# Kernel tuning notes

Measured on AMD Instinct MI355X. Metric: run time of the kernel, lower is better.

## Reference

```python
import jax, jax.numpy as jnp
import numpy as np

# Pauli-Z expectation table: sign of bit w in 4-bit index (wire 0 = MSB, axis order q0..q3)
_idx = np.arange(16)
_bits = (_idx[None, :] >> (3 - np.arange(4))[:, None]) & 1
_Z_TABLE = (1.0 - 2.0 * _bits).astype(np.float32)  # (4, 16)


def _apply_ry(state, theta, wire):
    # state: (N, 2,2,2,2) real amplitudes; RY = [[c,-s],[s,c]], c=cos(t/2), s=sin(t/2)
    ax = 1 + wire
    c = jnp.cos(theta / 2)
    s = jnp.sin(theta / 2)
    st = jnp.moveaxis(state, ax, 1)
    s0, s1 = st[:, 0], st[:, 1]
    st = jnp.stack([c * s0 - s * s1, s * s0 + c * s1], axis=1)
    return jnp.moveaxis(st, 1, ax)


def _apply_cnot(state, control, target):
    # flips the target axis on the control==1 slice (assumes target > control)
    ac, at = 1 + control, 1 + target
    s0 = jnp.take(state, 0, axis=ac)
    s1 = jnp.flip(jnp.take(state, 1, axis=ac), axis=at - 1)
    return jnp.stack([s0, s1], axis=ac)


def setup_inputs() -> dict:
    key = jax.random.key(0)
    ks = jax.random.split(key, 8)
    B = 8192
    x = jax.random.uniform(ks[0], (B, 1, 28, 28), dtype=jnp.float32)
    conv_w = jax.random.normal(ks[1], (4, 1, 2, 2), dtype=jnp.float32) * 0.5
    conv_b = jax.random.normal(ks[2], (4,), dtype=jnp.float32) * 0.1
    bn_gamma = jnp.ones((4,), jnp.float32)
    bn_beta = jnp.zeros((4,), jnp.float32)
    bn_mean = jnp.zeros((4,), jnp.float32)
    bn_var = jnp.ones((4,), jnp.float32)
    shortcut_weight = jnp.float32(1.0)
    theta = jax.random.normal(ks[3], (8,), dtype=jnp.float32)  # 8 trainable RY angles
    lin_w = jax.random.normal(ks[4], (10, 784), dtype=jnp.float32) * 0.03
    lin_b = jnp.zeros((10,), jnp.float32)
    log_scale = jnp.float32(1.0)
    return {"x": x, "conv_w": conv_w, "conv_b": conv_b, "bn_gamma": bn_gamma,
            "bn_beta": bn_beta, "bn_mean": bn_mean, "bn_var": bn_var,
            "shortcut_weight": shortcut_weight, "theta": theta,
            "lin_w": lin_w, "lin_b": lin_b, "log_scale": log_scale}


def reference(x, conv_w, conv_b, bn_gamma, bn_beta, bn_mean, bn_var,
              shortcut_weight, theta, lin_w, lin_b, log_scale):
    B = x.shape[0]
    # classical shortcut: conv(1->4, k2, s2) + BN (eval mode, running stats)
    sc = jax.lax.conv_general_dilated(
        x, conv_w, window_strides=(2, 2), padding='VALID',
        dimension_numbers=('NCHW', 'OIHW', 'NCHW')) + conv_b[None, :, None, None]
    sc = (sc - bn_mean[None, :, None, None]) * jax.lax.rsqrt(bn_var[None, :, None, None] + 1e-5)
    sc = sc * bn_gamma[None, :, None, None] + bn_beta[None, :, None, None]
    sc = sc.reshape(B, -1)  # (B, 784) channel-major, matches torch .view

    # extract 2x2 patches in (r, c) scan order -> (B*196, 4) with order [tl, tr, bl, br]
    img = x.reshape(B, 28, 28)
    patches = img.reshape(B, 14, 2, 14, 2).transpose(0, 1, 3, 2, 4).reshape(B * 196, 4)

    # RY encoding of |0000>: product state, amplitudes [cos(v/2), sin(v/2)] per wire
    half = patches * 0.5
    e = jnp.stack([jnp.cos(half), jnp.sin(half)], axis=-1)  # (N, 4, 2)
    state = jnp.einsum('na,nb,nc,nd->nabcd', e[:, 0], e[:, 1], e[:, 2], e[:, 3])

    # parameterized circuit: RY layer, CNOT(0,1), CNOT(2,3), RY layer
    for w in range(4):
        state = _apply_ry(state, theta[w], w)
    state = _apply_cnot(state, 0, 1)
    state = _apply_cnot(state, 2, 3)
    for w in range(4):
        state = _apply_ry(state, theta[4 + w], w)

    # <Z_w> expectations (real amplitudes -> probs = state**2)
    probs = (state ** 2).reshape(-1, 16)        # (B*196, 16)
    meas = probs @ jnp.asarray(_Z_TABLE).T      # (B*196, 4)
    qfeat = meas.reshape(B, 196 * 4)            # cat order: patch-major, wires inner

    feat = shortcut_weight * sc + qfeat
    logits = (feat @ lin_w.T + lin_b) * log_scale  # dropout is identity in eval
    return jax.nn.log_softmax(logits, axis=-1)
```

## Files before the change

kernel.cpp:

```cpp
#include <hip/hip_runtime.h>
#include <hip/hip_fp16.h>
#include <math.h>

#define BLOCK 256
#define WAVES 4
#define IPW   2
#define LWS   792
#define FEATS 792

typedef _Float16 h2v __attribute__((ext_vector_type(2)));

__device__ __forceinline__ float dot2h(unsigned a, unsigned b, float c) {
#if __has_builtin(__builtin_amdgcn_fdot2)
    return __builtin_amdgcn_fdot2(__builtin_bit_cast(h2v, a),
                                  __builtin_bit_cast(h2v, b), c, false);
#else
    h2v xa = __builtin_bit_cast(h2v, a), yb = __builtin_bit_cast(h2v, b);
    return c + (float)xa[0] * (float)yb[0] + (float)xa[1] * (float)yb[1];
#endif
}

__device__ __forceinline__ unsigned packh(float a, float b) {
    __half2 h = __float22half2_rn(make_float2(a, b));
    return __builtin_bit_cast(unsigned, h);
}

__global__ __launch_bounds__(BLOCK) void quanv_fused2(
    const float* __restrict__ x,
    const float* __restrict__ conv_w,
    const float* __restrict__ conv_b,
    const float* __restrict__ bn_gamma,
    const float* __restrict__ bn_beta,
    const float* __restrict__ bn_mean,
    const float* __restrict__ bn_var,
    const float* __restrict__ sw_p,
    const float* __restrict__ theta,
    const float* __restrict__ lin_w,
    const float* __restrict__ lin_b,
    const float* __restrict__ log_scale_p,
    float* __restrict__ out)
{
    __shared__ __half lw[10 * LWS];
    __shared__ __half feat[WAVES][FEATS];

    const int t = threadIdx.x;
    const int lane = t & 63, wv = t >> 6;
    __half* fw = &feat[wv][0];

    for (int g = t * 4; g < 7840; g += BLOCK * 4) {
        float4 v = *(const float4*)(lin_w + g);
        int k = g / 784, f = g - k * 784;
        uint2 pk;
        pk.x = packh(v.x, v.y);
        pk.y = packh(v.z, v.w);
        *(uint2*)&lw[k * LWS + f] = pk;
    }

    const float sw = sw_p[0];
    const float ls = log_scale_p[0];
    float wf[4][4], bf[4];
#pragma unroll
    for (int c = 0; c < 4; ++c) {
        float scale = bn_gamma[c] * rsqrtf(bn_var[c] + 1e-5f);
        float sws = sw * scale;
#pragma unroll
        for (int k = 0; k < 4; ++k) wf[c][k] = sws * conv_w[c * 4 + k];
        bf[c] = sw * (scale * (conv_b[c] - bn_mean[c]) + bn_beta[c]);
    }
    const float th0 = theta[0], th1 = theta[1], th2 = theta[2], th3 = theta[3];
    float s4, c4, s5, c5, s6, c6, s7, c7;
    __sincosf(0.5f * theta[4], &s4, &c4);
    __sincosf(0.5f * theta[5], &s5, &c5);
    __sincosf(0.5f * theta[6], &s6, &c6);
    __sincosf(0.5f * theta[7], &s7, &c7);

    auto pair_meas = [&](float xa, float xb, float tha, float thb,
                         float sE, float cE, float sF, float cF,
                         float& mA, float& mB) {
        float sA, cA, sB, cB;
        __sincosf(0.5f * (xa + tha), &sA, &cA);
        __sincosf(0.5f * (xb + thb), &sB, &cB);
        float cc = cA * cB, ss = sA * sB, cs = cA * sB, sc_ = sA * cB;
        float u0 = cE * cc - sE * ss;
        float u1 = cE * cs - sE * sc_;
        float u2 = sE * cc + cE * ss;
        float u3 = sE * cs + cE * sc_;
        float v0 = cF * u0 - sF * u1, v1 = sF * u0 + cF * u1;
        float v2 = cF * u2 - sF * u3, v3 = sF * u2 + cF * u3;
        mA = u0 * u0 + u1 * u1 - u2 * u2 - u3 * u3;
        mB = v0 * v0 - v1 * v1 + v2 * v2 - v3 * v3;
    };

    float2 px[8];
    auto load_pix = [&](int img) {
        const float* xb = x + (size_t)img * 784;
#pragma unroll
        for (int j = 0; j < 4; ++j) {
            int p = lane + 64 * j; if (p > 195) p = 195;
            int i = p / 14, jj = p - i * 14;
            px[2 * j]     = *(const float2*)(xb + (2 * i) * 28 + 2 * jj);
            px[2 * j + 1] = *(const float2*)(xb + (2 * i + 1) * 28 + 2 * jj);
        }
    };

    const int img0 = (blockIdx.x * WAVES + wv) * IPW;
    load_pix(img0);

    for (int it = 0; it < IPW; ++it) {
        const int img = img0 + it;
        unsigned q0[4], q1[4];

#pragma unroll
        for (int j = 0; j < 3; ++j) {
            const int p = lane + 64 * j;
            float x00 = px[2 * j].x, x01 = px[2 * j].y;
            float x10 = px[2 * j + 1].x, x11 = px[2 * j + 1].y;
            float m0, m1, m2, m3;
            pair_meas(x00, x01, th0, th1, s4, c4, s5, c5, m0, m1);
            pair_meas(x10, x11, th2, th3, s6, c6, s7, c7, m2, m3);
            q0[j] = packh(m0, m1);
            q1[j] = packh(m2, m3);
#pragma unroll
            for (int c = 0; c < 4; ++c)
                fw[c * 196 + p] = __float2half(
                    wf[c][0] * x00 + wf[c][1] * x01 +
                    wf[c][2] * x10 + wf[c][3] * x11 + bf[c]);
        }
        if (lane < 4) {
            const int p = lane + 192;
            float x00 = px[6].x, x01 = px[6].y;
            float x10 = px[7].x, x11 = px[7].y;
            float m0, m1, m2, m3;
            pair_meas(x00, x01, th0, th1, s4, c4, s5, c5, m0, m1);
            pair_meas(x10, x11, th2, th3, s6, c6, s7, c7, m2, m3);
            q0[3] = packh(m0, m1);
            q1[3] = packh(m2, m3);
#pragma unroll
            for (int c = 0; c < 4; ++c)
                fw[c * 196 + p] = __float2half(
                    wf[c][0] * x00 + wf[c][1] * x01 +
                    wf[c][2] * x10 + wf[c][3] * x11 + bf[c]);
        }

        if (it + 1 < IPW) load_pix(img + 1);

        __syncthreads();

#pragma unroll
        for (int j = 0; j < 3; ++j) {
            const int p = lane + 64 * j;
            uint2 v = *(uint2*)&fw[4 * p];
            __half2 a0 = __builtin_bit_cast(__half2, v.x);
            __half2 a1 = __builtin_bit_cast(__half2, v.y);
            a0 = __hadd2(a0, __builtin_bit_cast(__half2, q0[j]));
            a1 = __hadd2(a1, __builtin_bit_cast(__half2, q1[j]));
            v.x = __builtin_bit_cast(unsigned, a0);
            v.y = __builtin_bit_cast(unsigned, a1);
            *(uint2*)&fw[4 * p] = v;
        }
        if (lane < 4) {
            const int p = lane + 192;
            uint2 v = *(uint2*)&fw[4 * p];
            __half2 a0 = __builtin_bit_cast(__half2, v.x);
            __half2 a1 = __builtin_bit_cast(__half2, v.y);
            a0 = __hadd2(a0, __builtin_bit_cast(__half2, q0[3]));
            a1 = __hadd2(a1, __builtin_bit_cast(__half2, q1[3]));
            v.x = __builtin_bit_cast(unsigned, a0);
            v.y = __builtin_bit_cast(unsigned, a1);
            *(uint2*)&fw[4 * p] = v;
        }

        __syncthreads();

        float acc = 0.f;
        if (lane < 60) {
            const int k = lane / 6, c = lane - k * 6;
            const int start = c * 136;
            const int nit = (c == 5) ? 13 : 17;
            const uint4* fp = (const uint4*)&fw[start];
            const uint4* wp = (const uint4*)&lw[k * LWS + start];
            for (int i = 0; i < nit; ++i) {
                uint4 a = fp[i], b = wp[i];
                acc = dot2h(a.x, b.x, acc);
                acc = dot2h(a.y, b.y, acc);
                acc = dot2h(a.z, b.z, acc);
                acc = dot2h(a.w, b.w, acc);
            }
        }
        float s1 = acc + __shfl_down(acc, 1);
        float s2 = s1 + __shfl_down(s1, 2);
        float tot = s2 + __shfl_down(s1, 4);

        float logit = 0.f;
        if (lane < 60 && lane % 6 == 0)
            logit = (tot + lin_b[lane / 6]) * ls;

        float m = -1e30f;
        float lg;
#pragma unroll
        for (int kk = 0; kk < 10; ++kk) {
            float v = __shfl(logit, kk * 6);
            m = fmaxf(m, v);
        }
        float ssum = 0.f;
#pragma unroll
        for (int kk = 0; kk < 10; ++kk) {
            float v = __shfl(logit, kk * 6);
            ssum += __expf(v - m);
        }
        const float lse = m + __logf(ssum);
        lg = __shfl(logit, 6 * lane);
        if (lane < 10) out[(size_t)img * 10 + lane] = lg - lse;

        __syncthreads();
    }
}

extern "C" void kernel_launch(void* const* d_in, const int* in_sizes, int n_in,
                              void* d_out, int out_size, void* d_ws, size_t ws_size,
                              hipStream_t stream) {
    const float* x         = (const float*)d_in[0];
    const float* conv_w    = (const float*)d_in[1];
    const float* conv_b    = (const float*)d_in[2];
    const float* bn_gamma  = (const float*)d_in[3];
    const float* bn_beta   = (const float*)d_in[4];
    const float* bn_mean   = (const float*)d_in[5];
    const float* bn_var    = (const float*)d_in[6];
    const float* sw        = (const float*)d_in[7];
    const float* theta     = (const float*)d_in[8];
    const float* lin_w     = (const float*)d_in[9];
    const float* lin_b     = (const float*)d_in[10];
    const float* log_scale = (const float*)d_in[11];
    float* out = (float*)d_out;

    const int B = in_sizes[0] / 784;
    dim3 grid(B / (WAVES * IPW)), block(BLOCK);
    hipLaunchKernelGGL(quanv_fused2, grid, block, 0, stream,
                       x, conv_w, conv_b, bn_gamma, bn_beta, bn_mean, bn_var,
                       sw, theta, lin_w, lin_b, log_scale, out);
}
```

Measured before the change: 19.99 us.

## Process both images per wave concurrently with one block barrier

Blocks grow to 8 waves, and each wave handles its two images in parallel rather than in a loop. Both images' pixels are loaded up front, before the lin_w staging, and each image gets its own shared feature buffer. The three block-wide barriers per image become a wave-local lgkmcnt wait plus a single __syncthreads. Weight reads from shared memory are reused across both images' dot products. The aim is to cut barrier stalls and serialized latency, at the cost of more registers and shared memory per block, which may reduce occupancy.

```diff
diff --git a/kernel.cpp b/kernel.cpp
--- a/kernel.cpp
+++ b/kernel.cpp
@@ -2,9 +2,8 @@
 #include <hip/hip_fp16.h>
 #include <math.h>
 
-#define BLOCK 256
-#define WAVES 4
-#define IPW   2
+#define BLOCK 512
+#define WVS   8
 #define LWS   792
 #define FEATS 792
 
@@ -25,7 +24,9 @@
     return __builtin_bit_cast(unsigned, h);
 }
 
-__global__ __launch_bounds__(BLOCK) void quanv_fused2(
+#define WAVE_LGKM() asm volatile("s_waitcnt lgkmcnt(0)" ::: "memory")
+
+__global__ __launch_bounds__(BLOCK, 4) void quanv_fused3(
     const float* __restrict__ x,
     const float* __restrict__ conv_w,
     const float* __restrict__ conv_b,
@@ -41,11 +42,31 @@
     float* __restrict__ out)
 {
     __shared__ __half lw[10 * LWS];
-    __shared__ __half feat[WAVES][FEATS];
+    __shared__ __half feat[WVS][2][FEATS];
 
     const int t = threadIdx.x;
     const int lane = t & 63, wv = t >> 6;
-    __half* fw = &feat[wv][0];
+    __half* fw0 = &feat[wv][0][0];
+    __half* fw1 = &feat[wv][1][0];
+
+    const int img0 = (blockIdx.x * WVS + wv) * 2;
+    const int img1 = img0 + 1;
+
+    float2 px0[8], px1[8];
+    {
+        const float* xb0 = x + (size_t)img0 * 784;
+        const float* xb1 = x + (size_t)img1 * 784;
+#pragma unroll
+        for (int j = 0; j < 4; ++j) {
+            int p = lane + 64 * j; if (p > 195) p = 195;
+            int i = p / 14, jj = p - i * 14;
+            const int o0 = (2 * i) * 28 + 2 * jj, o1 = o0 + 28;
+            px0[2 * j]     = *(const float2*)(xb0 + o0);
+            px0[2 * j + 1] = *(const float2*)(xb0 + o1);
+            px1[2 * j]     = *(const float2*)(xb1 + o0);
+            px1[2 * j + 1] = *(const float2*)(xb1 + o1);
+        }
+    }
 
     for (int g = t * 4; g < 7840; g += BLOCK * 4) {
         float4 v = *(const float4*)(lin_w + g);
@@ -91,25 +112,8 @@
         mB = v0 * v0 - v1 * v1 + v2 * v2 - v3 * v3;
     };
 
-    float2 px[8];
-    auto load_pix = [&](int img) {
-        const float* xb = x + (size_t)img * 784;
-#pragma unroll
-        for (int j = 0; j < 4; ++j) {
-            int p = lane + 64 * j; if (p > 195) p = 195;
-            int i = p / 14, jj = p - i * 14;
-            px[2 * j]     = *(const float2*)(xb + (2 * i) * 28 + 2 * jj);
-            px[2 * j + 1] = *(const float2*)(xb + (2 * i + 1) * 28 + 2 * jj);
-        }
-    };
-
-    const int img0 = (blockIdx.x * WAVES + wv) * IPW;
-    load_pix(img0);
-
-    for (int it = 0; it < IPW; ++it) {
-        const int img = img0 + it;
-        unsigned q0[4], q1[4];
-
+    unsigned qa0[4], qa1[4], qb0[4], qb1[4];
+    auto pass1 = [&](const float2* px, __half* fw, unsigned* q0, unsigned* q1) {
 #pragma unroll
         for (int j = 0; j < 3; ++j) {
             const int p = lane + 64 * j;
@@ -141,13 +145,16 @@
                     wf[c][0] * x00 + wf[c][1] * x01 +
                     wf[c][2] * x10 + wf[c][3] * x11 + bf[c]);
         }
-
-        if (it + 1 < IPW) load_pix(img + 1);
-
-        __syncthreads();
-
-#pragma unroll
-        for (int j = 0; j < 3; ++j) {
+    };
+    pass1(px0, fw0, qa0, qa1);
+    pass1(px1, fw1, qb0, qb1);
+
+    WAVE_LGKM();
+
+    auto pass2 = [&](__half* fw, const unsigned* q0, const unsigned* q1) {
+#pragma unroll
+        for (int j = 0; j < 4; ++j) {
+            if (j == 3 && lane >= 4) break;
             const int p = lane + 64 * j;
             uint2 v = *(uint2*)&fw[4 * p];
             __half2 a0 = __builtin_bit_cast(__half2, v.x);
@@ -158,61 +165,66 @@
             v.y = __builtin_bit_cast(unsigned, a1);
             *(uint2*)&fw[4 * p] = v;
         }
-        if (lane < 4) {
-            const int p = lane + 192;
-            uint2 v = *(uint2*)&fw[4 * p];
-            __half2 a0 = __builtin_bit_cast(__half2, v.x);
-            __half2 a1 = __builtin_bit_cast(__half2, v.y);
-            a0 = __hadd2(a0, __builtin_bit_cast(__half2, q0[3]));
-            a1 = __hadd2(a1, __builtin_bit_cast(__half2, q1[3]));
-            v.x = __builtin_bit_cast(unsigned, a0);
-            v.y = __builtin_bit_cast(unsigned, a1);
-            *(uint2*)&fw[4 * p] = v;
-        }
-
-        __syncthreads();
-
-        float acc = 0.f;
-        if (lane < 60) {
-            const int k = lane / 6, c = lane - k * 6;
-            const int start = c * 136;
-            const int nit = (c == 5) ? 13 : 17;
-            const uint4* fp = (const uint4*)&fw[start];
-            const uint4* wp = (const uint4*)&lw[k * LWS + start];
-            for (int i = 0; i < nit; ++i) {
-                uint4 a = fp[i], b = wp[i];
-                acc = dot2h(a.x, b.x, acc);
-                acc = dot2h(a.y, b.y, acc);
-                acc = dot2h(a.z, b.z, acc);
-                acc = dot2h(a.w, b.w, acc);
-            }
-        }
-        float s1 = acc + __shfl_down(acc, 1);
-        float s2 = s1 + __shfl_down(s1, 2);
-        float tot = s2 + __shfl_down(s1, 4);
-
-        float logit = 0.f;
-        if (lane < 60 && lane % 6 == 0)
-            logit = (tot + lin_b[lane / 6]) * ls;
-
-        float m = -1e30f;
-        float lg;
-#pragma unroll
-        for (int kk = 0; kk < 10; ++kk) {
-            float v = __shfl(logit, kk * 6);
-            m = fmaxf(m, v);
-        }
-        float ssum = 0.f;
-#pragma unroll
-        for (int kk = 0; kk < 10; ++kk) {
-            float v = __shfl(logit, kk * 6);
-            ssum += __expf(v - m);
-        }
-        const float lse = m + __logf(ssum);
-        lg = __shfl(logit, 6 * lane);
-        if (lane < 10) out[(size_t)img * 10 + lane] = lg - lse;
-
-        __syncthreads();
+    };
+    pass2(fw0, qa0, qa1);
+    pass2(fw1, qb0, qb1);
+
+    __syncthreads();
+
+    float acc0 = 0.f, acc1 = 0.f;
+    if (lane < 60) {
+        const int k = lane / 6, c = lane - k * 6;
+        const int start = c * 136;
+        const int nit = (c == 5) ? 13 : 17;
+        const uint4* wp = (const uint4*)&lw[k * LWS + start];
+        const uint4* f0 = (const uint4*)&fw0[start];
+        const uint4* f1 = (const uint4*)&fw1[start];
+        for (int i = 0; i < nit; ++i) {
+            uint4 w = wp[i], a = f0[i], b = f1[i];
+            acc0 = dot2h(a.x, w.x, acc0);
+            acc0 = dot2h(a.y, w.y, acc0);
+            acc0 = dot2h(a.z, w.z, acc0);
+            acc0 = dot2h(a.w, w.w, acc0);
+            acc1 = dot2h(b.x, w.x, acc1);
+            acc1 = dot2h(b.y, w.y, acc1);
+            acc1 = dot2h(b.z, w.z, acc1);
+            acc1 = dot2h(b.w, w.w, acc1);
+        }
+    }
+
+    float s1a = acc0 + __shfl_down(acc0, 1);
+    float s2a = s1a + __shfl_down(s1a, 2);
+    float ta  = s2a + __shfl_down(s1a, 4);
+    float s1b = acc1 + __shfl_down(acc1, 1);
+    float s2b = s1b + __shfl_down(s1b, 2);
+    float tb  = s2b + __shfl_down(s1b, 4);
+
+    float logit0 = 0.f, logit1 = 0.f;
+    if (lane < 60 && lane % 6 == 0) {
+        const float bk = lin_b[lane / 6];
+        logit0 = (ta + bk) * ls;
+        logit1 = (tb + bk) * ls;
+    }
+
+    float m0 = -1e30f, m1 = -1e30f;
+#pragma unroll
+    for (int kk = 0; kk < 10; ++kk) {
+        m0 = fmaxf(m0, __shfl(logit0, kk * 6));
+        m1 = fmaxf(m1, __shfl(logit1, kk * 6));
+    }
+    float ss0 = 0.f, ss1 = 0.f;
+#pragma unroll
+    for (int kk = 0; kk < 10; ++kk) {
+        ss0 += __expf(__shfl(logit0, kk * 6) - m0);
+        ss1 += __expf(__shfl(logit1, kk * 6) - m1);
+    }
+    const float lse0 = m0 + __logf(ss0);
+    const float lse1 = m1 + __logf(ss1);
+    const float lg0 = __shfl(logit0, 6 * lane);
+    const float lg1 = __shfl(logit1, 6 * lane);
+    if (lane < 10) {
+        out[(size_t)img0 * 10 + lane] = lg0 - lse0;
+        out[(size_t)img1 * 10 + lane] = lg1 - lse1;
     }
 }
 
@@ -234,8 +246,8 @@
     float* out = (float*)d_out;
 
     const int B = in_sizes[0] / 784;
-    dim3 grid(B / (WAVES * IPW)), block(BLOCK);
-    hipLaunchKernelGGL(quanv_fused2, grid, block, 0, stream,
+    dim3 grid(B / (WVS * 2)), block(BLOCK);
+    hipLaunchKernelGGL(quanv_fused3, grid, block, 0, stream,
                        x, conv_w, conv_b, bn_gamma, bn_beta, bn_mean, bn_var,
                        sw, theta, lin_w, lin_b, log_scale, out);
 }
```

Measured after the change: 19.47 us. 2.6% less time.
